# Kernel optimization log

Measured on AMD Instinct MI355X. Metric: run time of the kernel, lower is better.

The kernel has to match this reference:

```python
import jax, jax.numpy as jnp
import numpy as np

E = 1024  # embedding_dim
A = 1024  # attention_dim


def setup_inputs() -> dict:
    key = jax.random.key(0)
    k0, k1, k2, k3 = jax.random.split(key, 4)
    embedded = jax.random.normal(k0, (4, 4096, E), dtype=jnp.float32)
    # torch Linear weight is [out, in]; stored here as [in, out] for x @ W
    scale = 1.0 / np.sqrt(E)
    Wk = jax.random.uniform(k1, (E, A), dtype=jnp.float32, minval=-scale, maxval=scale)
    Wq = jax.random.uniform(k2, (E, A), dtype=jnp.float32, minval=-scale, maxval=scale)
    Wv = jax.random.uniform(k3, (E, A), dtype=jnp.float32, minval=-scale, maxval=scale)
    return {"embedded": embedded, "Wk": Wk, "Wq": Wq, "Wv": Wv}


def reference(embedded, Wk, Wq, Wv):
    B, T, C = embedded.shape
    K = embedded @ Wk  # [B,T,A]
    Q = embedded @ Wq
    V = embedded @ Wv
    d_k = Q.shape[-1]
    scores = jnp.einsum('bqa,bka->bqk', Q, K) / jnp.sqrt(jnp.float32(d_k))
    causal = jnp.tril(jnp.ones((T, T), dtype=bool))
    scores = jnp.where(causal, scores, -jnp.inf)
    attn = jax.nn.softmax(scores, axis=-1)
    out = jnp.einsum('bqk,bka->bqa', attn, V)
    return jnp.round(out, decimals=4)
```

## Files before the change

kernel.cpp:

```cpp
#include <hip/hip_runtime.h>
#include <hip/hip_fp16.h>

#define T_SEQ 4096
#define NBATCH 4
#define EDIM 1024
#define ADIM 1024
#define MTOT (NBATCH * T_SEQ)

typedef _Float16 f16x8 __attribute__((ext_vector_type(8)));
typedef float f32x4 __attribute__((ext_vector_type(4)));

__global__ __launch_bounds__(256) void cast_transpose_w(
    const float* __restrict__ Wk, const float* __restrict__ Wq,
    const float* __restrict__ Wv, _Float16* __restrict__ Wt) {
  __shared__ float tile[32][33];
  const int z = blockIdx.z;
  const float* W = (z == 0) ? Wk : (z == 1) ? Wq : Wv;
  const int n0 = blockIdx.x * 32, k0 = blockIdx.y * 32;
  const int tx = threadIdx.x, ty = threadIdx.y;
#pragma unroll
  for (int yy = 0; yy < 32; yy += 8)
    tile[ty + yy][tx] = W[(size_t)(k0 + ty + yy) * ADIM + n0 + tx];
  __syncthreads();
  _Float16* out = Wt + (size_t)z * EDIM * ADIM;
#pragma unroll
  for (int yy = 0; yy < 32; yy += 8)
    out[(size_t)(n0 + ty + yy) * EDIM + k0 + tx] = (_Float16)tile[tx][ty + yy];
}

__global__ __launch_bounds__(256) void gemm_qkv(
    const float* __restrict__ X, const _Float16* __restrict__ Wt,
    _Float16* __restrict__ Qb, _Float16* __restrict__ Kb,
    _Float16* __restrict__ Vt) {
  const int z = blockIdx.z;
  const _Float16* Bt = Wt + (size_t)z * EDIM * ADIM;
  __shared__ __align__(16) _Float16 Al[128 * 32];
  __shared__ __align__(16) _Float16 Bl[128 * 32];
  const int tid = threadIdx.x;
  const int lane = tid & 63, w = tid >> 6;
  const int wm = w >> 1, wn = w & 1;
  const int lr = lane & 15, g = lane >> 4;
  const int m0 = blockIdx.y * 128, n0 = blockIdx.x * 128;
  const int arow = tid >> 1;
  const int ahalf = tid & 1;

  f32x4 acc[4][4] = {};

  for (int k0 = 0; k0 < EDIM; k0 += 32) {
    {
      const float* src = X + (size_t)(m0 + arow) * EDIM + k0 + ahalf * 16;
      float4 v0 = ((const float4*)src)[0];
      float4 v1 = ((const float4*)src)[1];
      float4 v2 = ((const float4*)src)[2];
      float4 v3 = ((const float4*)src)[3];
      f16x8 pa = {(_Float16)v0.x, (_Float16)v0.y, (_Float16)v0.z, (_Float16)v0.w,
                  (_Float16)v1.x, (_Float16)v1.y, (_Float16)v1.z, (_Float16)v1.w};
      f16x8 pb = {(_Float16)v2.x, (_Float16)v2.y, (_Float16)v2.z, (_Float16)v2.w,
                  (_Float16)v3.x, (_Float16)v3.y, (_Float16)v3.z, (_Float16)v3.w};
      *(f16x8*)&Al[arow * 32 + ahalf * 16] = pa;
      *(f16x8*)&Al[arow * 32 + ahalf * 16 + 8] = pb;
    }
#pragma unroll
    for (int t = 0; t < 2; ++t) {
      const int r0 = (w * 2 + t) * 16;
      const _Float16* gsrc =
          Bt + (size_t)(n0 + r0 + (lane >> 2)) * EDIM + k0 + (lane & 3) * 8;
      __builtin_amdgcn_global_load_lds(
          (const __attribute__((address_space(1))) void*)gsrc,
          (__attribute__((address_space(3))) void*)&Bl[r0 * 32], 16, 0, 0);
    }
    __syncthreads();
    f16x8 af[4], bf[4];
#pragma unroll
    for (int i = 0; i < 4; i++)
      af[i] = *(const f16x8*)&Al[(wm * 64 + i * 16 + lr) * 32 + g * 8];
#pragma unroll
    for (int j = 0; j < 4; j++)
      bf[j] = *(const f16x8*)&Bl[(wn * 64 + j * 16 + lr) * 32 + g * 8];
#pragma unroll
    for (int i = 0; i < 4; i++)
#pragma unroll
      for (int j = 0; j < 4; j++)
        acc[i][j] = __builtin_amdgcn_mfma_f32_16x16x32_f16(af[i], bf[j], acc[i][j], 0, 0, 0);
    __syncthreads();
  }

#pragma unroll
  for (int i = 0; i < 4; i++)
#pragma unroll
    for (int j = 0; j < 4; j++)
#pragma unroll
      for (int r = 0; r < 4; r++) {
        const int row = m0 + wm * 64 + i * 16 + 4 * g + r;
        const int col = n0 + wn * 64 + j * 16 + lr;
        const _Float16 hv = (_Float16)acc[i][j][r];
        if (z == 0)
          Kb[(size_t)row * ADIM + col] = hv;
        else if (z == 1)
          Qb[(size_t)row * ADIM + col] = hv;
        else {
          const int b = row >> 12, tt = row & 4095;
          Vt[((size_t)b * ADIM + col) * T_SEQ + tt] = hv;
        }
      }
}

__global__ __launch_bounds__(256) void gemm_sqk(
    const _Float16* __restrict__ Qb, const _Float16* __restrict__ Kb,
    _Float16* __restrict__ Sb) {
  const int bj = blockIdx.x, bi = blockIdx.y, b = blockIdx.z;
  if (bj > bi) return;
  __shared__ __align__(16) _Float16 Al[128 * 32];
  __shared__ __align__(16) _Float16 Bl[128 * 32];
  const int tid = threadIdx.x;
  const int lane = tid & 63, w = tid >> 6;
  const int wm = w >> 1, wn = w & 1;
  const int lr = lane & 15, g = lane >> 4;
  const int m0 = bi * 128, n0 = bj * 128;
  const _Float16* A = Qb + (size_t)b * T_SEQ * ADIM;
  const _Float16* B = Kb + (size_t)b * T_SEQ * ADIM;

  f32x4 acc[4][4] = {};

  for (int k0 = 0; k0 < ADIM; k0 += 32) {
#pragma unroll
    for (int t = 0; t < 2; ++t) {
      const int r0 = (w * 2 + t) * 16;
      const _Float16* ga =
          A + (size_t)(m0 + r0 + (lane >> 2)) * ADIM + k0 + (lane & 3) * 8;
      __builtin_amdgcn_global_load_lds(
          (const __attribute__((address_space(1))) void*)ga,
          (__attribute__((address_space(3))) void*)&Al[r0 * 32], 16, 0, 0);
      const _Float16* gb =
          B + (size_t)(n0 + r0 + (lane >> 2)) * ADIM + k0 + (lane & 3) * 8;
      __builtin_amdgcn_global_load_lds(
          (const __attribute__((address_space(1))) void*)gb,
          (__attribute__((address_space(3))) void*)&Bl[r0 * 32], 16, 0, 0);
    }
    __syncthreads();
    f16x8 af[4], bf[4];
#pragma unroll
    for (int i = 0; i < 4; i++)
      af[i] = *(const f16x8*)&Al[(wm * 64 + i * 16 + lr) * 32 + g * 8];
#pragma unroll
    for (int j = 0; j < 4; j++)
      bf[j] = *(const f16x8*)&Bl[(wn * 64 + j * 16 + lr) * 32 + g * 8];
#pragma unroll
    for (int i = 0; i < 4; i++)
#pragma unroll
      for (int j = 0; j < 4; j++)
        acc[i][j] = __builtin_amdgcn_mfma_f32_16x16x32_f16(af[i], bf[j], acc[i][j], 0, 0, 0);
    __syncthreads();
  }

  _Float16* Srow = Sb + (size_t)b * T_SEQ * T_SEQ;
#pragma unroll
  for (int i = 0; i < 4; i++)
#pragma unroll
    for (int j = 0; j < 4; j++)
#pragma unroll
      for (int r = 0; r < 4; r++) {
        const int row = m0 + wm * 64 + i * 16 + 4 * g + r;
        const int col = n0 + wn * 64 + j * 16 + lr;
        Srow[(size_t)row * T_SEQ + col] = (_Float16)acc[i][j][r];
      }
}

__global__ __launch_bounds__(512) void softmax_rows(_Float16* __restrict__ S) {
  const int i = blockIdx.x, b = blockIdx.y;
  const int padded = ((i >> 7) + 1) << 7;
  const int tid = threadIdx.x;
  const int lane = tid & 63, w = tid >> 6;
  const int j0 = tid * 8;
  const bool active = j0 < padded;
  _Float16* row = S + ((size_t)b * T_SEQ + i) * T_SEQ;
  const float sm_scale = 0.03125f;

  float v[8];
  float m = -1e30f;
  if (active) {
    f16x8 x = *(const f16x8*)(row + j0);
#pragma unroll
    for (int jj = 0; jj < 8; jj++) {
      const float sv = (j0 + jj <= i) ? (float)x[jj] * sm_scale : -1e30f;
      v[jj] = sv;
      m = fmaxf(m, sv);
    }
  } else {
#pragma unroll
    for (int jj = 0; jj < 8; jj++) v[jj] = -1e30f;
  }
#pragma unroll
  for (int off = 1; off < 64; off <<= 1) m = fmaxf(m, __shfl_xor(m, off));
  __shared__ float redm[8], reds[8];
  if (lane == 0) redm[w] = m;
  __syncthreads();
#pragma unroll
  for (int ww = 0; ww < 8; ww++) m = fmaxf(m, redm[ww]);

  float s = 0.f;
#pragma unroll
  for (int jj = 0; jj < 8; jj++) {
    v[jj] = __expf(v[jj] - m);
    s += v[jj];
  }
#pragma unroll
  for (int off = 1; off < 64; off <<= 1) s += __shfl_xor(s, off);
  if (lane == 0) reds[w] = s;
  __syncthreads();
  s = 0.f;
#pragma unroll
  for (int ww = 0; ww < 8; ww++) s += reds[ww];
  const float inv = 1.f / s;

  if (active) {
    f16x8 o;
#pragma unroll
    for (int jj = 0; jj < 8; jj++) o[jj] = (_Float16)(v[jj] * inv);
    *(f16x8*)(row + j0) = o;
  }
}

__global__ __launch_bounds__(256) void gemm_pv(
    const _Float16* __restrict__ Pb, const _Float16* __restrict__ Vt,
    float* __restrict__ Out) {
  const int bx = blockIdx.x, by = blockIdx.y, b = blockIdx.z;
  __shared__ __align__(16) _Float16 Al[128 * 32];
  __shared__ __align__(16) _Float16 Bl[128 * 32];
  const int tid = threadIdx.x;
  const int lane = tid & 63, w = tid >> 6;
  const int wm = w >> 1, wn = w & 1;
  const int lr = lane & 15, g = lane >> 4;
  const int m0 = by * 128, n0 = bx * 128;
  const int kmax = (by + 1) * 128;
  const _Float16* A = Pb + (size_t)b * T_SEQ * T_SEQ;
  const _Float16* B = Vt + (size_t)b * ADIM * T_SEQ;

  f32x4 acc[4][4] = {};

  for (int k0 = 0; k0 < kmax; k0 += 32) {
#pragma unroll
    for (int t = 0; t < 2; ++t) {
      const int r0 = (w * 2 + t) * 16;
      const _Float16* ga =
          A + (size_t)(m0 + r0 + (lane >> 2)) * T_SEQ + k0 + (lane & 3) * 8;
      __builtin_amdgcn_global_load_lds(
          (const __attribute__((address_space(1))) void*)ga,
          (__attribute__((address_space(3))) void*)&Al[r0 * 32], 16, 0, 0);
      const _Float16* gb =
          B + (size_t)(n0 + r0 + (lane >> 2)) * T_SEQ + k0 + (lane & 3) * 8;
      __builtin_amdgcn_global_load_lds(
          (const __attribute__((address_space(1))) void*)gb,
          (__attribute__((address_space(3))) void*)&Bl[r0 * 32], 16, 0, 0);
    }
    __syncthreads();
    f16x8 af[4], bf[4];
#pragma unroll
    for (int i = 0; i < 4; i++)
      af[i] = *(const f16x8*)&Al[(wm * 64 + i * 16 + lr) * 32 + g * 8];
#pragma unroll
    for (int j = 0; j < 4; j++)
      bf[j] = *(const f16x8*)&Bl[(wn * 64 + j * 16 + lr) * 32 + g * 8];
#pragma unroll
    for (int i = 0; i < 4; i++)
#pragma unroll
      for (int j = 0; j < 4; j++)
        acc[i][j] = __builtin_amdgcn_mfma_f32_16x16x32_f16(af[i], bf[j], acc[i][j], 0, 0, 0);
    __syncthreads();
  }

#pragma unroll
  for (int i = 0; i < 4; i++)
#pragma unroll
    for (int j = 0; j < 4; j++)
#pragma unroll
      for (int r = 0; r < 4; r++) {
        const int row = m0 + wm * 64 + i * 16 + 4 * g + r;
        const int col = n0 + wn * 64 + j * 16 + lr;
        Out[((size_t)b * T_SEQ + row) * ADIM + col] = acc[i][j][r];
      }
}

extern "C" void kernel_launch(void* const* d_in, const int* in_sizes, int n_in,
                              void* d_out, int out_size, void* d_ws, size_t ws_size,
                              hipStream_t stream) {
  const float* X = (const float*)d_in[0];
  const float* Wk = (const float*)d_in[1];
  const float* Wq = (const float*)d_in[2];
  const float* Wv = (const float*)d_in[3];
  float* Out = (float*)d_out;

  char* ws = (char*)d_ws;
  const size_t WT_BYTES = (size_t)3 * EDIM * ADIM * 2;
  const size_t MAT_BYTES = (size_t)MTOT * ADIM * 2;
  _Float16* Wt = (_Float16*)ws;
  _Float16* Kb = (_Float16*)(ws + WT_BYTES);
  _Float16* Qb = (_Float16*)(ws + WT_BYTES + MAT_BYTES);
  _Float16* Vt = (_Float16*)(ws + WT_BYTES + 2 * MAT_BYTES);
  _Float16* Sb = (_Float16*)(ws + WT_BYTES + 3 * MAT_BYTES);

  cast_transpose_w<<<dim3(32, 32, 3), dim3(32, 8), 0, stream>>>(Wk, Wq, Wv, Wt);
  gemm_qkv<<<dim3(ADIM / 128, MTOT / 128, 3), dim3(256), 0, stream>>>(X, Wt, Qb, Kb, Vt);
  gemm_sqk<<<dim3(32, 32, NBATCH), dim3(256), 0, stream>>>(Qb, Kb, Sb);
  softmax_rows<<<dim3(T_SEQ, NBATCH), dim3(512), 0, stream>>>(Sb);
  gemm_pv<<<dim3(ADIM / 128, T_SEQ / 128, NBATCH), dim3(256), 0, stream>>>(Sb, Vt, Out);
}
```

Baseline: 696.4 us.

## Pre-cast X to fp16, reorder LDS staging layout, remap blocks for XCD locality

Adds a separate cast kernel that converts X to fp16, so the QKV GEMM can stage both operands with direct global-to-LDS loads instead of converting in registers. The LDS tile layout changes so each 16-row group is stored k-chunk-major, which gives contiguous fragment reads and is meant to reduce bank conflicts. All three GEMMs remap the block index so consecutive blocks land on the same XCD group, and the causal QK GEMM launches only lower-triangular tiles (528 per batch) instead of early-exiting half the grid. The cost is an extra pass over X and index-decoding overhead; Xh shares workspace with Sb, which is safe only because Sb is written after the QKV GEMM finishes.

```diff
diff --git a/kernel.cpp b/kernel.cpp
--- a/kernel.cpp
+++ b/kernel.cpp
@@ -9,6 +9,31 @@
 
 typedef _Float16 f16x8 __attribute__((ext_vector_type(8)));
 typedef float f32x4 __attribute__((ext_vector_type(4)));
+
+#define STAGE(SRC, LD, LDSARR)                                               \
+  {                                                                          \
+    _Pragma("unroll") for (int t = 0; t < 2; ++t) {                          \
+      const int rb = w * 2 + t;                                              \
+      const _Float16* gsrc =                                                 \
+          (SRC) + (size_t)(rb * 16 + (lane & 15)) * (LD) + (lane >> 4) * 8;  \
+      __builtin_amdgcn_global_load_lds(                                      \
+          (const __attribute__((address_space(1))) void*)gsrc,               \
+          (__attribute__((address_space(3))) void*)&LDSARR[rb * 512], 16,    \
+          0, 0);                                                             \
+    }                                                                        \
+  }
+
+#define FRAG(LDSARR, B4, G) (*(const f16x8*)&LDSARR[((B4) * 4 + (G)) * 128 + lr * 8])
+
+__global__ __launch_bounds__(256) void cast_x(const float* __restrict__ X,
+                                              _Float16* __restrict__ Xh) {
+  const size_t i = ((size_t)blockIdx.x * 256 + threadIdx.x) * 8;
+  float4 a = ((const float4*)(X + i))[0];
+  float4 b = ((const float4*)(X + i))[1];
+  f16x8 o = {(_Float16)a.x, (_Float16)a.y, (_Float16)a.z, (_Float16)a.w,
+             (_Float16)b.x, (_Float16)b.y, (_Float16)b.z, (_Float16)b.w};
+  *(f16x8*)(Xh + i) = o;
+}
 
 __global__ __launch_bounds__(256) void cast_transpose_w(
     const float* __restrict__ Wk, const float* __restrict__ Wq,
@@ -29,54 +54,32 @@
 }
 
 __global__ __launch_bounds__(256) void gemm_qkv(
-    const float* __restrict__ X, const _Float16* __restrict__ Wt,
+    const _Float16* __restrict__ Xh, const _Float16* __restrict__ Wt,
     _Float16* __restrict__ Qb, _Float16* __restrict__ Kb,
     _Float16* __restrict__ Vt) {
   const int z = blockIdx.z;
   const _Float16* Bt = Wt + (size_t)z * EDIM * ADIM;
-  __shared__ __align__(16) _Float16 Al[128 * 32];
-  __shared__ __align__(16) _Float16 Bl[128 * 32];
+  __shared__ __align__(16) _Float16 Al[4096];
+  __shared__ __align__(16) _Float16 Bl[4096];
   const int tid = threadIdx.x;
   const int lane = tid & 63, w = tid >> 6;
   const int wm = w >> 1, wn = w & 1;
   const int lr = lane & 15, g = lane >> 4;
-  const int m0 = blockIdx.y * 128, n0 = blockIdx.x * 128;
-  const int arow = tid >> 1;
-  const int ahalf = tid & 1;
+  const int h = blockIdx.y * gridDim.x + blockIdx.x;
+  const int orig = (h & 7) * 128 + (h >> 3);
+  const int m0 = (orig >> 3) * 128, n0 = (orig & 7) * 128;
 
   f32x4 acc[4][4] = {};
 
   for (int k0 = 0; k0 < EDIM; k0 += 32) {
-    {
-      const float* src = X + (size_t)(m0 + arow) * EDIM + k0 + ahalf * 16;
-      float4 v0 = ((const float4*)src)[0];
-      float4 v1 = ((const float4*)src)[1];
-      float4 v2 = ((const float4*)src)[2];
-      float4 v3 = ((const float4*)src)[3];
-      f16x8 pa = {(_Float16)v0.x, (_Float16)v0.y, (_Float16)v0.z, (_Float16)v0.w,
-                  (_Float16)v1.x, (_Float16)v1.y, (_Float16)v1.z, (_Float16)v1.w};
-      f16x8 pb = {(_Float16)v2.x, (_Float16)v2.y, (_Float16)v2.z, (_Float16)v2.w,
-                  (_Float16)v3.x, (_Float16)v3.y, (_Float16)v3.z, (_Float16)v3.w};
-      *(f16x8*)&Al[arow * 32 + ahalf * 16] = pa;
-      *(f16x8*)&Al[arow * 32 + ahalf * 16 + 8] = pb;
-    }
-#pragma unroll
-    for (int t = 0; t < 2; ++t) {
-      const int r0 = (w * 2 + t) * 16;
-      const _Float16* gsrc =
-          Bt + (size_t)(n0 + r0 + (lane >> 2)) * EDIM + k0 + (lane & 3) * 8;
-      __builtin_amdgcn_global_load_lds(
-          (const __attribute__((address_space(1))) void*)gsrc,
-          (__attribute__((address_space(3))) void*)&Bl[r0 * 32], 16, 0, 0);
-    }
+    STAGE(Xh + (size_t)m0 * EDIM + k0, EDIM, Al);
+    STAGE(Bt + (size_t)n0 * EDIM + k0, EDIM, Bl);
     __syncthreads();
     f16x8 af[4], bf[4];
 #pragma unroll
-    for (int i = 0; i < 4; i++)
-      af[i] = *(const f16x8*)&Al[(wm * 64 + i * 16 + lr) * 32 + g * 8];
-#pragma unroll
-    for (int j = 0; j < 4; j++)
-      bf[j] = *(const f16x8*)&Bl[(wn * 64 + j * 16 + lr) * 32 + g * 8];
+    for (int i = 0; i < 4; i++) af[i] = FRAG(Al, wm * 4 + i, g);
+#pragma unroll
+    for (int j = 0; j < 4; j++) bf[j] = FRAG(Bl, wn * 4 + j, g);
 #pragma unroll
     for (int i = 0; i < 4; i++)
 #pragma unroll
@@ -108,14 +111,19 @@
 __global__ __launch_bounds__(256) void gemm_sqk(
     const _Float16* __restrict__ Qb, const _Float16* __restrict__ Kb,
     _Float16* __restrict__ Sb) {
-  const int bj = blockIdx.x, bi = blockIdx.y, b = blockIdx.z;
-  if (bj > bi) return;
-  __shared__ __align__(16) _Float16 Al[128 * 32];
-  __shared__ __align__(16) _Float16 Bl[128 * 32];
+  __shared__ __align__(16) _Float16 Al[4096];
+  __shared__ __align__(16) _Float16 Bl[4096];
+  const int b = blockIdx.y;
   const int tid = threadIdx.x;
   const int lane = tid & 63, w = tid >> 6;
   const int wm = w >> 1, wn = w & 1;
   const int lr = lane & 15, g = lane >> 4;
+  const int h = blockIdx.x;
+  const int orig = (h & 7) * 66 + (h >> 3);
+  int bi = (int)((sqrtf(8.f * orig + 1.f) - 1.f) * 0.5f);
+  while ((bi + 1) * (bi + 2) / 2 <= orig) ++bi;
+  while (bi * (bi + 1) / 2 > orig) --bi;
+  const int bj = orig - bi * (bi + 1) / 2;
   const int m0 = bi * 128, n0 = bj * 128;
   const _Float16* A = Qb + (size_t)b * T_SEQ * ADIM;
   const _Float16* B = Kb + (size_t)b * T_SEQ * ADIM;
@@ -123,28 +131,14 @@
   f32x4 acc[4][4] = {};
 
   for (int k0 = 0; k0 < ADIM; k0 += 32) {
-#pragma unroll
-    for (int t = 0; t < 2; ++t) {
-      const int r0 = (w * 2 + t) * 16;
-      const _Float16* ga =
-          A + (size_t)(m0 + r0 + (lane >> 2)) * ADIM + k0 + (lane & 3) * 8;
-      __builtin_amdgcn_global_load_lds(
-          (const __attribute__((address_space(1))) void*)ga,
-          (__attribute__((address_space(3))) void*)&Al[r0 * 32], 16, 0, 0);
-      const _Float16* gb =
-          B + (size_t)(n0 + r0 + (lane >> 2)) * ADIM + k0 + (lane & 3) * 8;
-      __builtin_amdgcn_global_load_lds(
-          (const __attribute__((address_space(1))) void*)gb,
-          (__attribute__((address_space(3))) void*)&Bl[r0 * 32], 16, 0, 0);
-    }
+    STAGE(A + (size_t)m0 * ADIM + k0, ADIM, Al);
+    STAGE(B + (size_t)n0 * ADIM + k0, ADIM, Bl);
     __syncthreads();
     f16x8 af[4], bf[4];
 #pragma unroll
-    for (int i = 0; i < 4; i++)
-      af[i] = *(const f16x8*)&Al[(wm * 64 + i * 16 + lr) * 32 + g * 8];
-#pragma unroll
-    for (int j = 0; j < 4; j++)
-      bf[j] = *(const f16x8*)&Bl[(wn * 64 + j * 16 + lr) * 32 + g * 8];
+    for (int i = 0; i < 4; i++) af[i] = FRAG(Al, wm * 4 + i, g);
+#pragma unroll
+    for (int j = 0; j < 4; j++) bf[j] = FRAG(Bl, wn * 4 + j, g);
 #pragma unroll
     for (int i = 0; i < 4; i++)
 #pragma unroll
@@ -224,13 +218,16 @@
 __global__ __launch_bounds__(256) void gemm_pv(
     const _Float16* __restrict__ Pb, const _Float16* __restrict__ Vt,
     float* __restrict__ Out) {
-  const int bx = blockIdx.x, by = blockIdx.y, b = blockIdx.z;
-  __shared__ __align__(16) _Float16 Al[128 * 32];
-  __shared__ __align__(16) _Float16 Bl[128 * 32];
+  __shared__ __align__(16) _Float16 Al[4096];
+  __shared__ __align__(16) _Float16 Bl[4096];
+  const int b = blockIdx.y;
   const int tid = threadIdx.x;
   const int lane = tid & 63, w = tid >> 6;
   const int wm = w >> 1, wn = w & 1;
   const int lr = lane & 15, g = lane >> 4;
+  const int h = blockIdx.x;
+  const int orig = (h & 7) * 32 + (h >> 3);
+  const int by = orig >> 3, bx = orig & 7;
   const int m0 = by * 128, n0 = bx * 128;
   const int kmax = (by + 1) * 128;
   const _Float16* A = Pb + (size_t)b * T_SEQ * T_SEQ;
@@ -239,28 +236,14 @@
   f32x4 acc[4][4] = {};
 
   for (int k0 = 0; k0 < kmax; k0 += 32) {
-#pragma unroll
-    for (int t = 0; t < 2; ++t) {
-      const int r0 = (w * 2 + t) * 16;
-      const _Float16* ga =
-          A + (size_t)(m0 + r0 + (lane >> 2)) * T_SEQ + k0 + (lane & 3) * 8;
-      __builtin_amdgcn_global_load_lds(
-          (const __attribute__((address_space(1))) void*)ga,
-          (__attribute__((address_space(3))) void*)&Al[r0 * 32], 16, 0, 0);
-      const _Float16* gb =
-          B + (size_t)(n0 + r0 + (lane >> 2)) * T_SEQ + k0 + (lane & 3) * 8;
-      __builtin_amdgcn_global_load_lds(
-          (const __attribute__((address_space(1))) void*)gb,
-          (__attribute__((address_space(3))) void*)&Bl[r0 * 32], 16, 0, 0);
-    }
+    STAGE(A + (size_t)m0 * T_SEQ + k0, T_SEQ, Al);
+    STAGE(B + (size_t)n0 * T_SEQ + k0, T_SEQ, Bl);
     __syncthreads();
     f16x8 af[4], bf[4];
 #pragma unroll
-    for (int i = 0; i < 4; i++)
-      af[i] = *(const f16x8*)&Al[(wm * 64 + i * 16 + lr) * 32 + g * 8];
-#pragma unroll
-    for (int j = 0; j < 4; j++)
-      bf[j] = *(const f16x8*)&Bl[(wn * 64 + j * 16 + lr) * 32 + g * 8];
+    for (int i = 0; i < 4; i++) af[i] = FRAG(Al, wm * 4 + i, g);
+#pragma unroll
+    for (int j = 0; j < 4; j++) bf[j] = FRAG(Bl, wn * 4 + j, g);
 #pragma unroll
     for (int i = 0; i < 4; i++)
 #pragma unroll
@@ -297,11 +280,13 @@
   _Float16* Kb = (_Float16*)(ws + WT_BYTES);
   _Float16* Qb = (_Float16*)(ws + WT_BYTES + MAT_BYTES);
   _Float16* Vt = (_Float16*)(ws + WT_BYTES + 2 * MAT_BYTES);
+  _Float16* Xh = (_Float16*)(ws + WT_BYTES + 3 * MAT_BYTES);
   _Float16* Sb = (_Float16*)(ws + WT_BYTES + 3 * MAT_BYTES);
 
+  cast_x<<<dim3(MTOT * EDIM / 2048), dim3(256), 0, stream>>>(X, Xh);
   cast_transpose_w<<<dim3(32, 32, 3), dim3(32, 8), 0, stream>>>(Wk, Wq, Wv, Wt);
-  gemm_qkv<<<dim3(ADIM / 128, MTOT / 128, 3), dim3(256), 0, stream>>>(X, Wt, Qb, Kb, Vt);
-  gemm_sqk<<<dim3(32, 32, NBATCH), dim3(256), 0, stream>>>(Qb, Kb, Sb);
+  gemm_qkv<<<dim3(8, 128, 3), dim3(256), 0, stream>>>(Xh, Wt, Qb, Kb, Vt);
+  gemm_sqk<<<dim3(528, NBATCH), dim3(256), 0, stream>>>(Qb, Kb, Sb);
   softmax_rows<<<dim3(T_SEQ, NBATCH), dim3(512), 0, stream>>>(Sb);
-  gemm_pv<<<dim3(ADIM / 128, T_SEQ / 128, NBATCH), dim3(256), 0, stream>>>(Sb, Vt, Out);
-}
+  gemm_pv<<<dim3(256, NBATCH), dim3(256), 0, stream>>>(Sb, Vt, Out);
+}
```

Result: slower. 823.4 us (+18.2%).
